# Kernel optimization log

Hardware: AMD Instinct MI355X
Metric: run time of the kernel (lower is better)

Reference implementation:

```python
import jax, jax.numpy as jnp
import numpy as np

TOPK = 2

def setup_inputs() -> dict:
    key = jax.random.key(0)
    ks = jax.random.split(key, 5)
    B, S, D, H, E = 2, 4096, 1024, 2048, 8
    x = jax.random.normal(ks[0], (B, S, D), dtype=jnp.float32)
    router_w = jax.random.normal(ks[1], (E, D), dtype=jnp.float32) * 0.02
    w1 = jax.random.normal(ks[2], (E, D, H), dtype=jnp.float32) * 0.02
    w3 = jax.random.normal(ks[3], (E, D, H), dtype=jnp.float32) * 0.02
    w2 = jax.random.normal(ks[4], (E, H, D), dtype=jnp.float32) * 0.02
    return {"x": x, "router_w": router_w, "w1": w1, "w3": w3, "w2": w2}

def reference(x, router_w, w1, w3, w2):
    B, S, D = x.shape
    E = router_w.shape[0]
    xf = x.reshape(-1, D)                      # [T, D]
    T = xf.shape[0]
    logits = (xf @ router_w.T).astype(jnp.float32)      # [T, E]
    weights, indices = jax.lax.top_k(logits, TOPK)      # [T, k]
    weights = jax.nn.softmax(weights, axis=-1).astype(x.dtype)
    prob = jax.nn.softmax(logits, axis=-1)              # [T, E] fp32
    P = prob.mean(axis=0).astype(x.dtype)               # [E]
    mask = jnp.zeros((T, E), jnp.float32).at[jnp.arange(T)[:, None], indices].set(1.0)
    f = mask.mean(axis=0).astype(x.dtype)               # [E]
    aux_loss = E * jnp.sum(f * P)
    out = jnp.zeros_like(xf)
    for e in range(E):
        # combine weight for expert e per token (0 if not routed here)
        coef = jnp.sum(jnp.where(indices == e, weights, jnp.zeros_like(weights)), axis=-1)  # [T]
        h = jax.nn.silu(xf @ w1[e]) * (xf @ w3[e])      # [T, H] SwiGLU
        out = out + coef[:, None] * (h @ w2[e])         # masked combine == gather/scatter
    return out.reshape(B, S, D), aux_loss
```

## Files before the change

### kernel.cpp

```cpp
#include <hip/hip_runtime.h>
#include <hip/hip_bf16.h>

#define TT 8192
#define DD 1024
#define HH 2048
#define EE 8

typedef __bf16 bf16x8 __attribute__((ext_vector_type(8)));
typedef float floatx4 __attribute__((ext_vector_type(4)));
typedef short shortx8 __attribute__((ext_vector_type(8)));

__device__ __forceinline__ short f2bf(float f) {
  unsigned u = __float_as_uint(f);
  u += 0x7fffu + ((u >> 16) & 1u);
  return (short)(u >> 16);
}

__device__ __forceinline__ void gld16(const void* g, void* l) {
  __builtin_amdgcn_global_load_lds((const __attribute__((address_space(1))) void*)g,
                                   (__attribute__((address_space(3))) void*)l, 16, 0, 0);
}

__global__ __launch_bounds__(256) void router_kernel(
    const float* __restrict__ x, const float* __restrict__ rw,
    int* __restrict__ cpad, float* __restrict__ ppad,
    int* __restrict__ list_token, float* __restrict__ list_coef,
    short* __restrict__ xb)
{
  __shared__ int   sE0[32], sE1[32], lcnt[EE], sbase[EE], lp0[32], lp1[32];
  __shared__ float sG0[32], sG1[32], sP[EE];
  const int tid = threadIdx.x;
  if (tid < EE) { sP[tid] = 0.f; lcnt[tid] = 0; }
  __syncthreads();
  const int lane = tid & 63, wv = tid >> 6;
  const int t0 = blockIdx.x * 32;
  for (int ti = 0; ti < 8; ++ti) {
    const int s = wv * 8 + ti;
    const int t = t0 + s;
    float sc[EE];
#pragma unroll
    for (int e = 0; e < EE; ++e) sc[e] = 0.f;
#pragma unroll
    for (int j = 0; j < 4; ++j) {
      float4 xv = *(const float4*)(x + (size_t)t * DD + j * 256 + lane * 4);
#pragma unroll
      for (int e = 0; e < EE; ++e) {
        float4 rv = *(const float4*)(rw + e * DD + j * 256 + lane * 4);
        sc[e] += xv.x * rv.x + xv.y * rv.y + xv.z * rv.z + xv.w * rv.w;
      }
      if (xb) {
        short4 sv = make_short4(f2bf(xv.x), f2bf(xv.y), f2bf(xv.z), f2bf(xv.w));
        *(short4*)(xb + (size_t)t * DD + j * 256 + lane * 4) = sv;
      }
    }
#pragma unroll
    for (int off = 32; off > 0; off >>= 1)
#pragma unroll
      for (int e = 0; e < EE; ++e)
        sc[e] += __shfl_down(sc[e], off);
    if (lane == 0) {
      int i0 = 0; float l0 = sc[0];
      for (int e = 1; e < EE; ++e) if (sc[e] > l0) { l0 = sc[e]; i0 = e; }
      int i1 = -1; float l1 = -3.4e38f;
      for (int e = 0; e < EE; ++e) if (e != i0 && sc[e] > l1) { l1 = sc[e]; i1 = e; }
      const float g0 = 1.f / (1.f + __expf(l1 - l0));
      float pr[EE]; float sum = 0.f;
      for (int e = 0; e < EE; ++e) { pr[e] = __expf(sc[e] - l0); sum += pr[e]; }
      const float inv = 1.f / sum;
      for (int e = 0; e < EE; ++e) atomicAdd(&sP[e], pr[e] * inv);
      sE0[s] = i0; sE1[s] = i1; sG0[s] = g0; sG1[s] = 1.f - g0;
    }
  }
  __syncthreads();
  if (tid < 32) {
    lp0[tid] = atomicAdd(&lcnt[sE0[tid]], 1);
    lp1[tid] = atomicAdd(&lcnt[sE1[tid]], 1);
  }
  __syncthreads();
  if (tid < EE) {
    sbase[tid] = atomicAdd(&cpad[tid * 16], lcnt[tid]);
    atomicAdd(&ppad[tid * 16], sP[tid]);
  }
  __syncthreads();
  if (tid < 32) {
    int e0 = sE0[tid], e1 = sE1[tid], t = t0 + tid;
    int p0 = sbase[e0] + lp0[tid];
    int p1 = sbase[e1] + lp1[tid];
    list_token[e0 * TT + p0] = t; list_coef[e0 * TT + p0] = sG0[tid];
    list_token[e1 * TT + p1] = t; list_coef[e1 * TT + p1] = sG1[tid];
  }
}

__global__ void aux_kernel(const int* __restrict__ cpad, const float* __restrict__ ppad,
                           int* __restrict__ offsets, float* __restrict__ out_aux)
{
  if (threadIdx.x == 0) {
    float aux = 0.f; int off = 0;
    for (int e = 0; e < EE; ++e) {
      aux += ((float)cpad[e * 16] / (float)TT) * (ppad[e * 16] / (float)TT);
      offsets[e] = off; off += cpad[e * 16];
    }
    *out_aux = aux * (float)EE;
  }
}

__global__ __launch_bounds__(256) void convt_kernel(const float* __restrict__ in, short* __restrict__ out,
                                                    int R, int C, int mode)
{
  __shared__ short T[64 * 74];
  const int t = threadIdx.x;
  in  += (size_t)blockIdx.z * R * C;
  out += (size_t)blockIdx.z * R * C * (mode ? 2 : 1);
  const int c0 = blockIdx.x * 64, r0 = blockIdx.y * 64;
#pragma unroll
  for (int p = 0; p < 4; ++p) {
    int r = p * 16 + (t >> 4), c4 = (t & 15) * 4;
    float4 v = *(const float4*)(in + (size_t)(r0 + r) * C + c0 + c4);
    short4 s = make_short4(f2bf(v.x), f2bf(v.y), f2bf(v.z), f2bf(v.w));
    *(short4*)&T[r * 74 + c4] = s;
  }
  __syncthreads();
#pragma unroll
  for (int q = 0; q < 2; ++q) {
    int u = q * 256 + t;
    int oc = u >> 3, k8 = (u & 7) * 8;
    shortx8 s;
#pragma unroll
    for (int j = 0; j < 8; ++j) s[j] = T[(k8 + j) * 74 + oc];
    int c = c0 + oc;
    int grow = (mode == 0) ? c : (2 * (c & ~31) + (c & 31) + ((mode == 2) ? 32 : 0));
    *(shortx8*)&out[(size_t)grow * R + r0 + k8] = s;
  }
}


#define PH_BAR()  { __builtin_amdgcn_s_barrier(); __builtin_amdgcn_sched_barrier(0); }
#define WAITL0()  { asm volatile("s_waitcnt lgkmcnt(0)" ::: "memory"); __builtin_amdgcn_sched_barrier(0); }
#define WAITVN(n) { asm volatile("s_waitcnt vmcnt(" #n ")" ::: "memory"); __builtin_amdgcn_sched_barrier(0); }

template<int NT>
__device__ __forceinline__ void mma_core(char* SM, int tid,
    const char* a00, const char* a01, const char* a10, const char* a11,
    const char* b00, const char* b01, const char* b10, const char* b11,
    floatx4 (&acc)[8][4])
{
  const int lane = tid & 63, w = tid >> 6;
  const int l16 = lane & 15, quad = lane >> 4;
  const int wm = (w >> 2) & 1, wn = w & 3;
  const int cx = (((l16 >> 1) & 1) << 4) | (((l16 >> 2) & 1) << 5) | ((l16 & 1) << 6);
  const int ck0 = (quad * 16) ^ cx;
  const int arb = (wm * 128 + l16) * 128;
  const int brb = 32768 + (wn * 64 + l16) * 128;
  const int wq = w * 2048;

#define SA_(u,h,p0,p1) { gld16((p0) + (size_t)(u) * 128, SM + (((u) & 1) << 16) + (h) * 16384 + wq); \
                         gld16((p1) + (size_t)(u) * 128, SM + (((u) & 1) << 16) + (h) * 16384 + wq + 1024); }
#define SB_(u,h,p0,p1) { gld16((p0) + (size_t)(u) * 128, SM + (((u) & 1) << 16) + 32768 + (h) * 16384 + wq); \
                         gld16((p1) + (size_t)(u) * 128, SM + (((u) & 1) << 16) + 32768 + (h) * 16384 + wq + 1024); }
#define LA_(mi) { a[mi][0] = *(const bf16x8*)(SM + cur + arb + (mi) * 2048 + ck0); \
                  a[mi][1] = *(const bf16x8*)(SM + cur + arb + (mi) * 2048 + (ck0 ^ 64)); }
#define LB_(ni) { b[ni][0] = *(const bf16x8*)(SM + cur + brb + (ni) * 2048 + ck0); \
                  b[ni][1] = *(const bf16x8*)(SM + cur + brb + (ni) * 2048 + (ck0 ^ 64)); }
#define MM_(mi,ni) { acc[mi][ni] = __builtin_amdgcn_mfma_f32_16x16x32_bf16(a[mi][0], b[ni][0], acc[mi][ni], 0, 0, 0); \
                     acc[mi][ni] = __builtin_amdgcn_mfma_f32_16x16x32_bf16(a[mi][1], b[ni][1], acc[mi][ni], 0, 0, 0); }

  SA_(0, 0, a00, a01); SA_(0, 1, a10, a11);
  SB_(0, 0, b00, b01); SB_(0, 1, b10, b11);
  SA_(1, 0, a00, a01); SA_(1, 1, a10, a11);
  WAITVN(4);
  __builtin_amdgcn_s_barrier();
  __builtin_amdgcn_sched_barrier(0);

#pragma unroll 2
  for (int t = 0; t < NT; ++t) {
    const int cur = (t & 1) << 16;
    bf16x8 a[8][2], b[4][2];
    LA_(0) LA_(1) LA_(2) LA_(3) LB_(0) LB_(1)
    if (t + 1 < NT) SB_(t + 1, 0, b00, b01);
    PH_BAR(); WAITL0();
    __builtin_amdgcn_s_setprio(1);
    MM_(0,0) MM_(1,0) MM_(2,0) MM_(3,0) MM_(0,1) MM_(1,1) MM_(2,1) MM_(3,1)
    __builtin_amdgcn_s_setprio(0);
    PH_BAR();
    LA_(4) LA_(5) LA_(6) LA_(7) LB_(2) LB_(3)
    if (t + 1 < NT) SB_(t + 1, 1, b10, b11);
    PH_BAR(); WAITL0();
    __builtin_amdgcn_s_setprio(1);
    MM_(4,2) MM_(5,2) MM_(6,2) MM_(7,2) MM_(4,3) MM_(5,3) MM_(6,3) MM_(7,3)
    __builtin_amdgcn_s_setprio(0);
    PH_BAR();
    if (t + 2 < NT) SA_(t + 2, 0, a00, a01);
    PH_BAR();
    __builtin_amdgcn_s_setprio(1);
    MM_(0,2) MM_(1,2) MM_(2,2) MM_(3,2) MM_(0,3) MM_(1,3) MM_(2,3) MM_(3,3)
    __builtin_amdgcn_s_setprio(0);
    PH_BAR();
    if (t + 2 < NT) SA_(t + 2, 1, a10, a11);
    PH_BAR();
    __builtin_amdgcn_s_setprio(1);
    MM_(4,0) MM_(5,0) MM_(6,0) MM_(7,0) MM_(4,1) MM_(5,1) MM_(6,1) MM_(7,1)
    __builtin_amdgcn_s_setprio(0);
    if (t + 2 < NT) { WAITVN(4); } else { WAITVN(0); }
    PH_BAR();
  }
#undef SA_
#undef SB_
#undef LA_
#undef LB_
#undef MM_
}

__global__ __launch_bounds__(512, 2) void g1p_kernel(
    const short* __restrict__ xb, const short* __restrict__ w13t,
    const int* __restrict__ cpad, const int* __restrict__ offsets,
    const int* __restrict__ list_token, short* __restrict__ Hbuf)
{
  const int e = blockIdx.z, rb = blockIdx.y, nb = blockIdx.x;
  const int cnt = cpad[e * 16];
  if (rb * 256 >= cnt) return;
  __shared__ char SM[131072];
  const int tid = threadIdx.x;
  const int lane = tid & 63, w = tid >> 6;
  const int srow = lane >> 3;
  const int scol = (((lane ^ (lane >> 4)) & 1) << 4)
                 | ((((lane >> 1) ^ (lane >> 5)) & 1) << 5)
                 | ((((lane >> 2) ^ (lane >> 3)) & 1) << 6);
  const int* lt = list_token + e * TT;
  const char* ap[2][2];
#pragma unroll
  for (int h = 0; h < 2; ++h)
#pragma unroll
    for (int i = 0; i < 2; ++i) {
      int gr = rb * 256 + h * 128 + (w * 2 + i) * 8 + srow;
      int tok = (gr < cnt) ? lt[gr] : lt[0];
      ap[h][i] = (const char*)xb + (size_t)tok * 2048 + scol;
    }
  const char* bb = (const char*)w13t + ((size_t)e * 4096 + nb * 256) * 2048
                 + (size_t)(w * 16 + srow) * 2048 + scol;
  floatx4 acc[8][4] = {};
  mma_core<16>(SM, tid, ap[0][0], ap[0][1], ap[1][0], ap[1][1],
               bb, bb + 8 * 2048, bb + 128 * 2048, bb + 136 * 2048, acc);
  const int off = offsets[e];
  const int l16 = lane & 15, quad = lane >> 4;
  const int wm = (w >> 2) & 1, wn = w & 3;
#pragma unroll
  for (int mi = 0; mi < 8; ++mi)
#pragma unroll
    for (int r = 0; r < 4; ++r) {
      int grow = rb * 256 + wm * 128 + mi * 16 + quad * 4 + r;
      if (grow < cnt) {
        size_t rowbase = (size_t)(off + grow) * HH + nb * 128 + wn * 32;
#pragma unroll
        for (int ni = 0; ni < 2; ++ni) {
          float aa = acc[mi][ni][r], bbv = acc[mi][ni + 2][r];
          float hv = aa / (1.f + __expf(-aa)) * bbv;
          Hbuf[rowbase + ni * 16 + l16] = f2bf(hv);
        }
      }
    }
}

__global__ __launch_bounds__(512, 2) void g2p_kernel(
    const short* __restrict__ Hbuf, const short* __restrict__ w2t,
    const int* __restrict__ cpad, const int* __restrict__ offsets,
    const int* __restrict__ list_token, const float* __restrict__ list_coef,
    float* __restrict__ out)
{
  const int e = blockIdx.z, rb = blockIdx.y, nb = blockIdx.x;
  const int cnt = cpad[e * 16];
  if (rb * 256 >= cnt) return;
  __shared__ char SM[131072];
  const int tid = threadIdx.x;
  const int lane = tid & 63, w = tid >> 6;
  const int srow = lane >> 3;
  const int scol = (((lane ^ (lane >> 4)) & 1) << 4)
                 | ((((lane >> 1) ^ (lane >> 5)) & 1) << 5)
                 | ((((lane >> 2) ^ (lane >> 3)) & 1) << 6);
  const int off = offsets[e];
  const char* ap[2][2];
#pragma unroll
  for (int h = 0; h < 2; ++h)
#pragma unroll
    for (int i = 0; i < 2; ++i) {
      int gr = rb * 256 + h * 128 + (w * 2 + i) * 8 + srow;
      int cg = (gr < cnt) ? gr : (cnt - 1);
      ap[h][i] = (const char*)Hbuf + (size_t)(off + cg) * 4096 + scol;
    }
  const char* bb = (const char*)w2t + ((size_t)e * DD + nb * 256) * 4096
                 + (size_t)(w * 16 + srow) * 4096 + scol;
  floatx4 acc[8][4] = {};
  mma_core<32>(SM, tid, ap[0][0], ap[0][1], ap[1][0], ap[1][1],
               bb, bb + 8 * 4096, bb + 128 * 4096, bb + 136 * 4096, acc);
  const int l16 = lane & 15, quad = lane >> 4;
  const int wm = (w >> 2) & 1, wn = w & 3;
#pragma unroll
  for (int mi = 0; mi < 8; ++mi)
#pragma unroll
    for (int r = 0; r < 4; ++r) {
      int grow = rb * 256 + wm * 128 + mi * 16 + quad * 4 + r;
      if (grow < cnt) {
        int tokid = list_token[e * TT + grow];
        float coef = list_coef[e * TT + grow];
        float* orow = out + (size_t)tokid * DD + nb * 256 + wn * 64;
#pragma unroll
        for (int ni = 0; ni < 4; ++ni)
          atomicAdd(&orow[ni * 16 + l16], coef * acc[mi][ni][r]);
      }
    }
}

__global__ __launch_bounds__(256, 2) void g1s_kernel(
    const float* __restrict__ x, const float* __restrict__ w1, const float* __restrict__ w3,
    const int* __restrict__ cpad, const int* __restrict__ offsets,
    const int* __restrict__ list_token, short* __restrict__ Hbuf)
{
  const int e = blockIdx.z, rb = blockIdx.y, nb = blockIdx.x;
  const int cnt = cpad[e * 16];
  if (rb * 128 >= cnt) return;
  __shared__ short Asm[128 * 40];
  __shared__ short B1sm[128 * 40];
  __shared__ short B3sm[128 * 40];
  const int tid = threadIdx.x, lane = tid & 63, wv = tid >> 6;
  const int wm = (wv >> 1) * 64, wn = (wv & 1) * 64;
  const int quad = lane >> 4, l16 = lane & 15;
  floatx4 acc1[4][4] = {{{0.f}}};
  floatx4 acc3[4][4] = {{{0.f}}};
  const int ar = tid >> 3, ak = (tid & 7) * 4;
  const int bp = tid & 63, bq = tid >> 6;
  const int bswz = (bq ^ ((bp >> 2) & 3)) * 8;
  const int bo0 = (2 * bp) * 40 + bswz, bo1 = bo0 + 40;
  int aro[4], bro[4];
#pragma unroll
  for (int mi = 0; mi < 4; ++mi) aro[mi] = (wm + mi * 16 + l16) * 40 + quad * 8;
#pragma unroll
  for (int ni = 0; ni < 4; ++ni) {
    int nl = wn + ni * 16 + l16;
    bro[ni] = nl * 40 + ((quad ^ ((nl >> 3) & 3)) * 8);
  }
  int tok[4];
#pragma unroll
  for (int i = 0; i < 4; ++i) {
    int gr = rb * 128 + ar + 32 * i;
    tok[i] = (gr < cnt) ? list_token[e * TT + gr] : list_token[e * TT];
  }
  const float* w1e = w1 + (size_t)e * DD * HH + (size_t)nb * 128;
  const float* w3e = w3 + (size_t)e * DD * HH + (size_t)nb * 128;
  for (int k0 = 0; k0 < DD; k0 += 32) {
    __syncthreads();
#pragma unroll
    for (int i = 0; i < 4; ++i) {
      int r = ar + 32 * i;
      float4 v = *(const float4*)(x + (size_t)tok[i] * DD + k0 + ak);
      short4 sv = make_short4(f2bf(v.x), f2bf(v.y), f2bf(v.z), f2bf(v.w));
      *(short4*)&Asm[r * 40 + ak] = sv;
    }
    {
      float2 u[8];
#pragma unroll
      for (int j = 0; j < 8; ++j) u[j] = *(const float2*)(w1e + (size_t)(k0 + bq * 8 + j) * HH + 2 * bp);
      shortx8 p0, p1;
#pragma unroll
      for (int j = 0; j < 8; ++j) { p0[j] = f2bf(u[j].x); p1[j] = f2bf(u[j].y); }
      *(shortx8*)&B1sm[bo0] = p0; *(shortx8*)&B1sm[bo1] = p1;
    }
    {
      float2 u[8];
#pragma unroll
      for (int j = 0; j < 8; ++j) u[j] = *(const float2*)(w3e + (size_t)(k0 + bq * 8 + j) * HH + 2 * bp);
      shortx8 p0, p1;
#pragma unroll
      for (int j = 0; j < 8; ++j) { p0[j] = f2bf(u[j].x); p1[j] = f2bf(u[j].y); }
      *(shortx8*)&B3sm[bo0] = p0; *(shortx8*)&B3sm[bo1] = p1;
    }
    __syncthreads();
    bf16x8 af[4], b1f[4], b3f[4];
#pragma unroll
    for (int mi = 0; mi < 4; ++mi) af[mi] = *(const bf16x8*)&Asm[aro[mi]];
#pragma unroll
    for (int ni = 0; ni < 4; ++ni) {
      b1f[ni] = *(const bf16x8*)&B1sm[bro[ni]];
      b3f[ni] = *(const bf16x8*)&B3sm[bro[ni]];
    }
#pragma unroll
    for (int mi = 0; mi < 4; ++mi)
#pragma unroll
      for (int ni = 0; ni < 4; ++ni) {
        acc1[mi][ni] = __builtin_amdgcn_mfma_f32_16x16x32_bf16(af[mi], b1f[ni], acc1[mi][ni], 0, 0, 0);
        acc3[mi][ni] = __builtin_amdgcn_mfma_f32_16x16x32_bf16(af[mi], b3f[ni], acc3[mi][ni], 0, 0, 0);
      }
  }
  const int off = offsets[e];
#pragma unroll
  for (int mi = 0; mi < 4; ++mi)
#pragma unroll
    for (int r = 0; r < 4; ++r) {
      int row = wm + mi * 16 + quad * 4 + r;
      int grow = rb * 128 + row;
      if (grow < cnt) {
        size_t rowbase = (size_t)(off + grow) * HH + (size_t)nb * 128 + wn;
#pragma unroll
        for (int ni = 0; ni < 4; ++ni) {
          float a = acc1[mi][ni][r], b = acc3[mi][ni][r];
          float h = a / (1.f + __expf(-a)) * b;
          Hbuf[rowbase + ni * 16 + l16] = f2bf(h);
        }
      }
    }
}

__global__ __launch_bounds__(256, 2) void g2s_kernel(
    const short* __restrict__ Hbuf, const float* __restrict__ w2,
    const int* __restrict__ cpad, const int* __restrict__ offsets,
    const int* __restrict__ list_token, const float* __restrict__ list_coef,
    float* __restrict__ out)
{
  const int e = blockIdx.z, rb = blockIdx.y, nb = blockIdx.x;
  const int cnt = cpad[e * 16];
  if (rb * 128 >= cnt) return;
  __shared__ short Asm[128 * 40];
  __shared__ short Bsm[128 * 40];
  const int tid = threadIdx.x, lane = tid & 63, wv = tid >> 6;
  const int wm = (wv >> 1) * 64, wn = (wv & 1) * 64;
  const int quad = lane >> 4, l16 = lane & 15;
  floatx4 acc[4][4] = {{{0.f}}};
  const int ar = tid >> 3, ak = (tid & 7) * 4;
  const int bp = tid & 63, bq = tid >> 6;
  const int bswz = (bq ^ ((bp >> 2) & 3)) * 8;
  const int bo0 = (2 * bp) * 40 + bswz, bo1 = bo0 + 40;
  int aro[4], bro[4];
#pragma unroll
  for (int mi = 0; mi < 4; ++mi) aro[mi] = (wm + mi * 16 + l16) * 40 + quad * 8;
#pragma unroll
  for (int ni = 0; ni < 4; ++ni) {
    int nl = wn + ni * 16 + l16;
    bro[ni] = nl * 40 + ((quad ^ ((nl >> 3) & 3)) * 8);
  }
  const int off = offsets[e];
  size_t hrow[4];
#pragma unroll
  for (int i = 0; i < 4; ++i) {
    int gr = rb * 128 + ar + 32 * i;
    int cg = (gr < cnt) ? gr : (cnt - 1);
    hrow[i] = (size_t)(off + cg) * HH;
  }
  const float* w2e = w2 + (size_t)e * HH * DD + (size_t)nb * 128;
  for (int k0 = 0; k0 < HH; k0 += 32) {
    __syncthreads();
#pragma unroll
    for (int i = 0; i < 4; ++i) {
      int r = ar + 32 * i;
      short4 sv = *(const short4*)(Hbuf + hrow[i] + k0 + ak);
      *(short4*)&Asm[r * 40 + ak] = sv;
    }
    {
      float2 u[8];
#pragma unroll
      for (int j = 0; j < 8; ++j) u[j] = *(const float2*)(w2e + (size_t)(k0 + bq * 8 + j) * DD + 2 * bp);
      shortx8 p0, p1;
#pragma unroll
      for (int j = 0; j < 8; ++j) { p0[j] = f2bf(u[j].x); p1[j] = f2bf(u[j].y); }
      *(shortx8*)&Bsm[bo0] = p0; *(shortx8*)&Bsm[bo1] = p1;
    }
    __syncthreads();
    bf16x8 af[4], bf[4];
#pragma unroll
    for (int mi = 0; mi < 4; ++mi) af[mi] = *(const bf16x8*)&Asm[aro[mi]];
#pragma unroll
    for (int ni = 0; ni < 4; ++ni) bf[ni] = *(const bf16x8*)&Bsm[bro[ni]];
#pragma unroll
    for (int mi = 0; mi < 4; ++mi)
#pragma unroll
      for (int ni = 0; ni < 4; ++ni)
        acc[mi][ni] = __builtin_amdgcn_mfma_f32_16x16x32_bf16(af[mi], bf[ni], acc[mi][ni], 0, 0, 0);
  }
#pragma unroll
  for (int mi = 0; mi < 4; ++mi)
#pragma unroll
    for (int r = 0; r < 4; ++r) {
      int row = wm + mi * 16 + quad * 4 + r;
      int grow = rb * 128 + row;
      if (grow < cnt) {
        int tokid = list_token[e * TT + grow];
        float coef = list_coef[e * TT + grow];
        float* orow = out + (size_t)tokid * DD + (size_t)nb * 128 + wn;
#pragma unroll
        for (int ni = 0; ni < 4; ++ni)
          atomicAdd(&orow[ni * 16 + l16], coef * acc[mi][ni][r]);
      }
    }
}

extern "C" void kernel_launch(void* const* d_in, const int* in_sizes, int n_in,
                              void* d_out, int out_size, void* d_ws, size_t ws_size,
                              hipStream_t stream)
{
  const float* x  = (const float*)d_in[0];
  const float* rw = (const float*)d_in[1];
  const float* w1 = (const float*)d_in[2];
  const float* w3 = (const float*)d_in[3];
  const float* w2 = (const float*)d_in[4];
  float* out = (float*)d_out;

  char* ws = (char*)d_ws;
  int*   cpad      = (int*)(ws + 0);
  float* ppad      = (float*)(ws + 512);
  int*   offsets   = (int*)(ws + 1024);
  int*   list_tok  = (int*)(ws + 4096);
  float* list_coef = (float*)(ws + 4096 + EE * TT * 4);

  const size_t OFF_W1T = 1u << 20;
  const size_t OFF_W3T = OFF_W1T + ((size_t)EE * DD * HH * 2);
  const size_t OFF_XBF = OFF_W3T + ((size_t)EE * DD * HH * 2);
  const size_t OFF_HB  = OFF_XBF + ((size_t)TT * DD * 2);
  const size_t NEED    = OFF_HB + ((size_t)(2 * TT + 128) * HH * 2);

  hipMemsetAsync(ws, 0, 1024, stream);
  hipMemsetAsync(d_out, 0, (size_t)TT * DD * sizeof(float), stream);

  const bool fast = (ws_size >= NEED);
  short* XBF = fast ? (short*)(ws + OFF_XBF) : nullptr;

  router_kernel<<<256, 256, 0, stream>>>(x, rw, cpad, ppad, list_tok, list_coef, XBF);
  aux_kernel<<<1, 64, 0, stream>>>(cpad, ppad, offsets, out + (size_t)TT * DD);

  if (fast) {
    short* W13T = (short*)(ws + OFF_W1T);
    short* HB   = (short*)(ws + OFF_HB);
    convt_kernel<<<dim3(HH / 64, DD / 64, EE), 256, 0, stream>>>(w1, W13T, DD, HH, 1);
    convt_kernel<<<dim3(HH / 64, DD / 64, EE), 256, 0, stream>>>(w3, W13T, DD, HH, 2);
    g1p_kernel<<<dim3(2 * HH / 256, TT / 256, EE), 512, 0, stream>>>(XBF, W13T, cpad, offsets, list_tok, HB);
    convt_kernel<<<dim3(DD / 64, HH / 64, EE), 256, 0, stream>>>(w2, W13T, HH, DD, 0);
    g2p_kernel<<<dim3(DD / 256, TT / 256, EE), 512, 0, stream>>>(HB, W13T, cpad, offsets, list_tok, list_coef, out);
  } else {
    short* HB = (short*)(ws + (1 << 20));
    g1s_kernel<<<dim3(HH / 128, TT / 128, EE), 256, 0, stream>>>(x, w1, w3, cpad, offsets, list_tok, HB);
    g2s_kernel<<<dim3(DD / 128, TT / 128, EE), 256, 0, stream>>>(HB, w2, cpad, offsets, list_tok, list_coef, out);
  }
}
```

Baseline: 626.1 us.

## Remap blocks to XCDs for L2 reuse and use smaller-tile down-projection GEMM

The first GEMM's block index is remapped so that blocks sharing the same weight column tiles land on the same XCD, aiming to improve L2 reuse across the chiplets. The second GEMM replaces the pipelined 256x256 mma_core kernel with a simpler 128x128 tile, 256-thread, single-buffered kernel that also uses XCD-aware block mapping. Each XCD owns one output column block of w2. The simpler kernel gives up the software pipelining and priority scheduling, so it may stall more on loads in exchange for more blocks and better locality.

```diff
diff --git a/kernel.cpp b/kernel.cpp
--- a/kernel.cpp
+++ b/kernel.cpp
@@ -215,7 +215,9 @@
     const int* __restrict__ cpad, const int* __restrict__ offsets,
     const int* __restrict__ list_token, short* __restrict__ Hbuf)
 {
-  const int e = blockIdx.z, rb = blockIdx.y, nb = blockIdx.x;
+  const int lin = blockIdx.x + 16 * (blockIdx.y + 32 * blockIdx.z);
+  const int xcd = lin & 7, c = lin >> 3;
+  const int e = c >> 6, rb = (c >> 1) & 31, nb = (xcd << 1) | (c & 1);
   const int cnt = cpad[e * 16];
   if (rb * 256 >= cnt) return;
   __shared__ char SM[131072];
@@ -260,48 +262,64 @@
     }
 }
 
-__global__ __launch_bounds__(512, 2) void g2p_kernel(
+__global__ __launch_bounds__(256, 2) void g2x_kernel(
     const short* __restrict__ Hbuf, const short* __restrict__ w2t,
     const int* __restrict__ cpad, const int* __restrict__ offsets,
     const int* __restrict__ list_token, const float* __restrict__ list_coef,
     float* __restrict__ out)
 {
-  const int e = blockIdx.z, rb = blockIdx.y, nb = blockIdx.x;
+  const int lin = blockIdx.x + 8 * (blockIdx.y + 64 * blockIdx.z);
+  const int xcd = lin & 7, c = lin >> 3;
+  const int nb = xcd, e = c >> 6, rb = c & 63;
   const int cnt = cpad[e * 16];
-  if (rb * 256 >= cnt) return;
-  __shared__ char SM[131072];
-  const int tid = threadIdx.x;
-  const int lane = tid & 63, w = tid >> 6;
-  const int srow = lane >> 3;
-  const int scol = (((lane ^ (lane >> 4)) & 1) << 4)
-                 | ((((lane >> 1) ^ (lane >> 5)) & 1) << 5)
-                 | ((((lane >> 2) ^ (lane >> 3)) & 1) << 6);
+  if (rb * 128 >= cnt) return;
+  __shared__ short Asm[128 * 32];
+  __shared__ short Bsm[128 * 32];
+  const int tid = threadIdx.x, lane = tid & 63, wv = tid >> 6;
+  const int wm = (wv >> 1) * 64, wn = (wv & 1) * 64;
+  const int quad = lane >> 4, l16 = lane & 15;
+  floatx4 acc[4][4] = {{{0.f}}};
   const int off = offsets[e];
-  const char* ap[2][2];
-#pragma unroll
-  for (int h = 0; h < 2; ++h)
-#pragma unroll
-    for (int i = 0; i < 2; ++i) {
-      int gr = rb * 256 + h * 128 + (w * 2 + i) * 8 + srow;
-      int cg = (gr < cnt) ? gr : (cnt - 1);
-      ap[h][i] = (const char*)Hbuf + (size_t)(off + cg) * 4096 + scol;
-    }
-  const char* bb = (const char*)w2t + ((size_t)e * DD + nb * 256) * 4096
-                 + (size_t)(w * 16 + srow) * 4096 + scol;
-  floatx4 acc[8][4] = {};
-  mma_core<32>(SM, tid, ap[0][0], ap[0][1], ap[1][0], ap[1][1],
-               bb, bb + 8 * 4096, bb + 128 * 4096, bb + 136 * 4096, acc);
-  const int l16 = lane & 15, quad = lane >> 4;
-  const int wm = (w >> 2) & 1, wn = w & 3;
-#pragma unroll
-  for (int mi = 0; mi < 8; ++mi)
+  const int qrow = wv * 32 + (lane >> 2);
+  const int qcb = (lane & 3) * 16;
+  const char* ag = (const char*)(Hbuf + (size_t)(off + rb * 128 + qrow) * HH) + qcb;
+  const char* bg = (const char*)(w2t + (size_t)e * DD * HH + (size_t)(nb * 128 + qrow) * HH) + qcb;
+  char* al = (char*)Asm + wv * 2048;
+  char* bl = (char*)Bsm + wv * 2048;
+  int aro[4], bro[4];
+#pragma unroll
+  for (int mi = 0; mi < 4; ++mi) aro[mi] = (wm + mi * 16 + l16) * 32 + quad * 8;
+#pragma unroll
+  for (int ni = 0; ni < 4; ++ni) bro[ni] = (wn + ni * 16 + l16) * 32 + quad * 8;
+
+  for (int k0 = 0; k0 < HH; k0 += 32) {
+    __syncthreads();
+    gld16(ag + (size_t)k0 * 2, al);
+    gld16(ag + (size_t)k0 * 2 + 16 * HH * 2, al + 1024);
+    gld16(bg + (size_t)k0 * 2, bl);
+    gld16(bg + (size_t)k0 * 2 + 16 * HH * 2, bl + 1024);
+    __syncthreads();
+    bf16x8 af[4], bf[4];
+#pragma unroll
+    for (int mi = 0; mi < 4; ++mi) af[mi] = *(const bf16x8*)&Asm[aro[mi]];
+#pragma unroll
+    for (int ni = 0; ni < 4; ++ni) bf[ni] = *(const bf16x8*)&Bsm[bro[ni]];
+#pragma unroll
+    for (int mi = 0; mi < 4; ++mi)
+#pragma unroll
+      for (int ni = 0; ni < 4; ++ni)
+        acc[mi][ni] = __builtin_amdgcn_mfma_f32_16x16x32_bf16(af[mi], bf[ni], acc[mi][ni], 0, 0, 0);
+  }
+#pragma unroll
+  for (int mi = 0; mi < 4; ++mi)
 #pragma unroll
     for (int r = 0; r < 4; ++r) {
-      int grow = rb * 256 + wm * 128 + mi * 16 + quad * 4 + r;
+      int row = wm + mi * 16 + quad * 4 + r;
+      int grow = rb * 128 + row;
       if (grow < cnt) {
         int tokid = list_token[e * TT + grow];
         float coef = list_coef[e * TT + grow];
-        float* orow = out + (size_t)tokid * DD + nb * 256 + wn * 64;
+        float* orow = out + (size_t)tokid * DD + (size_t)nb * 128 + wn;
 #pragma unroll
         for (int ni = 0; ni < 4; ++ni)
           atomicAdd(&orow[ni * 16 + l16], coef * acc[mi][ni][r]);
@@ -528,9 +546,9 @@
     short* HB   = (short*)(ws + OFF_HB);
     convt_kernel<<<dim3(HH / 64, DD / 64, EE), 256, 0, stream>>>(w1, W13T, DD, HH, 1);
     convt_kernel<<<dim3(HH / 64, DD / 64, EE), 256, 0, stream>>>(w3, W13T, DD, HH, 2);
-    g1p_kernel<<<dim3(2 * HH / 256, TT / 256, EE), 512, 0, stream>>>(XBF, W13T, cpad, offsets, list_tok, HB);
+    g1p_kernel<<<dim3(16, 32, EE), 512, 0, stream>>>(XBF, W13T, cpad, offsets, list_tok, HB);
     convt_kernel<<<dim3(DD / 64, HH / 64, EE), 256, 0, stream>>>(w2, W13T, HH, DD, 0);
-    g2p_kernel<<<dim3(DD / 256, TT / 256, EE), 512, 0, stream>>>(HB, W13T, cpad, offsets, list_tok, list_coef, out);
+    g2x_kernel<<<dim3(8, 64, EE), 256, 0, stream>>>(HB, W13T, cpad, offsets, list_tok, list_coef, out);
   } else {
     short* HB = (short*)(ws + (1 << 20));
     g1s_kernel<<<dim3(HH / 128, TT / 128, EE), 256, 0, stream>>>(x, w1, w3, cpad, offsets, list_tok, HB);
```

Measured after the change: 607.7 us. 1.03x faster.
